# Optimization experiments

Hardware: AMD Instinct MI355X
Metric: run time of the kernel (lower is better)

## Reference

```python
import jax, jax.numpy as jnp
import numpy as np

# Sizes (see shape_source): node irreps 32x0e + 16x1o, edge SH 1x1o,
# messages after concat/filter = 48x0e + 48x1o, MLP 16->64->64->96,
# final equivariant Linear -> 32x0e + 16x1o.
N, E = 50000, 800000
S_IN, V_IN, INV = 32, 16, 16
S_MSG, V_MSG = S_IN + V_IN, S_IN + V_IN  # 48, 48
NFAC = S_MSG + V_MSG                      # 96
S_OUT, V_OUT = 32, 16
SQRT3 = 3.0 ** 0.5


def setup_inputs() -> dict:
    key = jax.random.key(0)
    ks = jax.random.split(key, 12)
    return {
        "edge_src": jax.random.randint(ks[0], (E,), 0, N),
        "edge_dst": jax.random.randint(ks[1], (E,), 0, N),
        "edge_weight_cutoff": jax.random.uniform(ks[2], (E,), dtype=jnp.float32),
        "edge_inv": jax.random.normal(ks[3], (E, INV), dtype=jnp.float32),
        "node_scalars": jax.random.normal(ks[4], (N, S_IN), dtype=jnp.float32),
        "node_vectors": jax.random.normal(ks[5], (N, V_IN, 3), dtype=jnp.float32),
        "edge_sh_vec": jax.random.normal(ks[6], (E, 1, 3), dtype=jnp.float32),
        "W0": jax.random.normal(ks[7], (INV, 64), dtype=jnp.float32),
        "W1": jax.random.normal(ks[8], (64, 64), dtype=jnp.float32),
        "W2": jax.random.normal(ks[9], (64, NFAC), dtype=jnp.float32),
        "WL_s": jax.random.normal(ks[10], (S_MSG, S_OUT), dtype=jnp.float32),
        "WL_v": jax.random.normal(ks[11], (V_MSG, V_OUT), dtype=jnp.float32),
    }


def reference(edge_src, edge_dst, edge_weight_cutoff, edge_inv,
              node_scalars, node_vectors, edge_sh_vec,
              W0, W1, W2, WL_s, WL_v):
    # gather source-node features per edge
    src_s = node_scalars[edge_src]            # [E, 32]
    src_v = node_vectors[edge_src]            # [E, 16, 3]
    ev = edge_sh_vec[:, 0, :]                 # [E, 3] equivariant edge vector (1o)

    # equivariant tensor product (component-normalized CG paths):
    #   0e x 1o -> 1o : scalar * vector
    tp_v = src_s[:, :, None] * edge_sh_vec    # [E, 32, 3]
    #   1o x 1o -> 0e : dot / sqrt(3)   (1e, 2e outputs dropped by the output-irreps filter)
    tp_s = jnp.einsum('eci,ei->ec', src_v, ev) / SQRT3  # [E, 16]

    # concatenate with gathered node features and regroup by irrep
    msg_s = jnp.concatenate([tp_s, src_s], axis=-1)     # [E, 48] (0e block)
    msg_v = jnp.concatenate([tp_v, src_v], axis=1)      # [E, 48, 3] (1o block)

    # edge-conditioned gating MLP on invariant edge features (e3nn-normalized)
    h = jax.nn.silu(edge_inv @ W0 / jnp.sqrt(jnp.float32(INV)))
    h = jax.nn.silu(h @ W1 / jnp.sqrt(jnp.float32(64)))
    fac = h @ W2 / jnp.sqrt(jnp.float32(64))            # [E, 96]

    # elementwise tensor product with scalar factors + smooth cutoff
    g = fac * edge_weight_cutoff[:, None]
    msg_s = msg_s * g[:, :S_MSG]
    msg_v = msg_v * g[:, S_MSG:, None]

    # scatter-sum messages into destination nodes
    out_s = jax.ops.segment_sum(msg_s, edge_dst, num_segments=N)  # [N, 48]
    out_v = jax.ops.segment_sum(msg_v, edge_dst, num_segments=N)  # [N, 48, 3]

    # equivariant Linear to irreps_node_output (fan-in normalized)
    y_s = out_s @ WL_s / jnp.sqrt(jnp.float32(S_MSG))                       # [N, 32]
    y_v = jnp.einsum('eci,co->eoi', out_v, WL_v) / jnp.sqrt(jnp.float32(V_MSG))  # [N, 16, 3]

    # return as contiguous IrrepsArray storage [N, 32 + 16*3]
    return jnp.concatenate([y_s, y_v.reshape(y_v.shape[0], -1)], axis=-1)
```

## Files before the change

kernel.cpp:

```cpp
#include <hip/hip_runtime.h>
#include <hip/hip_fp16.h>
#include <math.h>

constexpr int S_IN = 32, V_IN = 16, INVD = 16;
constexpr int S_MSG = S_IN + V_IN;
constexpr int V_MSG = S_IN + V_IN;
constexpr int NFAC  = S_MSG + V_MSG;
constexpr int S_OUT = 32, V_OUT = 16;
constexpr int OUT_PER_NODE = S_OUT + V_OUT * 3;
constexpr float ISQRT3 = 0.57735026918962576f;
constexpr float ISQ48  = 0.14433756729740643f;

constexpr int PW0 = 0, PW1 = 2560, PW2 = 7168, PWL = 14080, PWTOT = 17536;

typedef _Float16 f16x8 __attribute__((ext_vector_type(8)));
typedef __attribute__((ext_vector_type(4))) float f32x4;

__device__ __forceinline__ float silu_f(float x) {
    return x * __builtin_amdgcn_rcpf(1.0f + __expf(-x));
}
__device__ __forceinline__ unsigned int hpack2(float a, float b) {
    __half2 h = __floats2half2_rn(a, b);
    return *reinterpret_cast<unsigned int*>(&h);
}
__device__ __forceinline__ unsigned short f2h(float f) {
    __half h = __float2half_rn(f);
    return __half_as_ushort(h);
}
__device__ __forceinline__ float h2f(unsigned short u) {
    return __half2float(__ushort_as_half(u));
}
__device__ __forceinline__ float lo16f(unsigned int u) { return h2f((unsigned short)(u & 0xffffu)); }
__device__ __forceinline__ float hi16f(unsigned int u) { return h2f((unsigned short)(u >> 16)); }
__device__ __forceinline__ unsigned int pkmul(unsigned int a, unsigned int b) {
    __half2 ha = *reinterpret_cast<__half2*>(&a);
    __half2 hb = *reinterpret_cast<__half2*>(&b);
    __half2 hc = __hmul2(ha, hb);
    return *reinterpret_cast<unsigned int*>(&hc);
}
__device__ __forceinline__ float2 up2(unsigned int u) {
    __half2 h = *reinterpret_cast<__half2*>(&u);
    return __half22float2(h);
}

__global__ __launch_bounds__(256) void hist_prep(
    const int* __restrict__ edst, int* __restrict__ deg, int E,
    const float* __restrict__ W0, const float* __restrict__ W1,
    const float* __restrict__ W2, const float* __restrict__ WLs,
    const float* __restrict__ WLv,
    const float* __restrict__ ns, const float* __restrict__ nv,
    unsigned short* __restrict__ pW,
    unsigned short* __restrict__ pNS,
    unsigned short* __restrict__ pNV,
    int Nn)
{
    int i = blockIdx.x * 256 + threadIdx.x;
    if (i < E) atomicAdd(&deg[edst[i]], 1);

    int nNS = Nn * 4;
    int nNV = Nn * 6;
    if (i < PWTOT) {
        float v = 0.0f;
        if (i < PW1) {
            int j = i / 40, k = i - 40 * j;
            if (k < INVD) v = W0[k * 64 + j];
        } else if (i < PW2) {
            int t = i - PW1; int j = t / 72, k = t - 72 * j;
            if (k < 64) v = W1[k * 64 + j];
        } else if (i < PWL) {
            int t = i - PW2; int j = t / 72, k = t - 72 * j;
            if (k < 64) v = W2[k * 96 + j];
        } else {
            int t = i - PWL; int j = t / 72, k = t - 72 * j;
            if (k < 48) v = (j < 32) ? WLs[k * S_OUT + j] : WLv[k * V_OUT + (j - 32)];
        }
        pW[i] = f2h(v);
    } else if (i < PWTOT + nNS) {
        int g = i - PWTOT;
        const float4* s4 = reinterpret_cast<const float4*>(ns + (size_t)g * 8);
        float4 a = s4[0], b = s4[1];
        *reinterpret_cast<uint4*>(pNS + (size_t)g * 8) =
            make_uint4(hpack2(a.x, a.y), hpack2(a.z, a.w), hpack2(b.x, b.y), hpack2(b.z, b.w));
    } else if (i < PWTOT + nNS + nNV) {
        int g = i - PWTOT - nNS;
        const float4* s4 = reinterpret_cast<const float4*>(nv + (size_t)g * 8);
        float4 a = s4[0], b = s4[1];
        *reinterpret_cast<uint4*>(pNV + (size_t)g * 8) =
            make_uint4(hpack2(a.x, a.y), hpack2(a.z, a.w), hpack2(b.x, b.y), hpack2(b.z, b.w));
    }
}

__global__ __launch_bounds__(256) void scanA(
    const int* __restrict__ deg, int* __restrict__ bsum, int Nn)
{
    __shared__ int sh[256];
    int i = blockIdx.x * 256 + threadIdx.x;
    sh[threadIdx.x] = (i < Nn) ? deg[i] : 0;
    __syncthreads();
    for (int o = 128; o > 0; o >>= 1) {
        if (threadIdx.x < o) sh[threadIdx.x] += sh[threadIdx.x + o];
        __syncthreads();
    }
    if (threadIdx.x == 0) bsum[blockIdx.x] = sh[0];
}

__global__ __launch_bounds__(1024) void scanB(int* __restrict__ bsum, int nb)
{
    __shared__ int sh[1024];
    int t = threadIdx.x;
    sh[t] = (t < nb) ? bsum[t] : 0;
    __syncthreads();
    for (int o = 1; o < 1024; o <<= 1) {
        int v = (t >= o) ? sh[t - o] : 0;
        __syncthreads();
        sh[t] += v;
        __syncthreads();
    }
    if (t < nb) bsum[t] = (t > 0) ? sh[t - 1] : 0;
}

__global__ __launch_bounds__(256) void scanC(
    const int* __restrict__ deg, const int* __restrict__ bsum,
    int* __restrict__ offs, int* __restrict__ cursor, int Nn, int E)
{
    __shared__ int sh[256];
    int i = blockIdx.x * 256 + threadIdx.x;
    int t = threadIdx.x;
    int v = (i < Nn) ? deg[i] : 0;
    sh[t] = v;
    __syncthreads();
    for (int o = 1; o < 256; o <<= 1) {
        int u = (t >= o) ? sh[t - o] : 0;
        __syncthreads();
        sh[t] += u;
        __syncthreads();
    }
    int excl = sh[t] - v + bsum[blockIdx.x];
    if (i < Nn) { offs[i] = excl; cursor[i] = excl; }
    if (i == Nn - 1) offs[Nn] = E;
}

__global__ __launch_bounds__(256) void scatter_permute(
    const int*   __restrict__ edst,
    const int*   __restrict__ esrc,
    const float* __restrict__ ecut,
    const float* __restrict__ esh,
    const float* __restrict__ einv,
    int* __restrict__ cursor,
    uint4* __restrict__ pedge,
    int E)
{
    int e = blockIdx.x * 256 + threadIdx.x;
    if (e >= E) return;
    int d = edst[e];
    int pos = atomicAdd(&cursor[d], 1);

    const float4* xr = reinterpret_cast<const float4*>(einv + (size_t)e * INVD);
    float4 a = xr[0], b = xr[1], c = xr[2], f = xr[3];
    uint4 r0 = make_uint4(hpack2(a.x, a.y), hpack2(a.z, a.w), hpack2(b.x, b.y), hpack2(b.z, b.w));
    uint4 r1 = make_uint4(hpack2(c.x, c.y), hpack2(c.z, c.w), hpack2(f.x, f.y), hpack2(f.z, f.w));
    uint4 r2 = make_uint4(hpack2(ecut[e], esh[(size_t)e * 3 + 0]),
                          hpack2(esh[(size_t)e * 3 + 1], esh[(size_t)e * 3 + 2]),
                          (unsigned int)esrc[e], (unsigned int)d);

    uint4* dst = pedge + (size_t)pos * 3;
    dst[0] = r0; dst[1] = r1; dst[2] = r2;
}

__global__ __launch_bounds__(256, 3) void edge_mega(
    const uint4* __restrict__ pedge,
    const unsigned short* __restrict__ pW,
    const unsigned short* __restrict__ pNS,
    const unsigned short* __restrict__ pNV,
    float* __restrict__ out,
    int E)
{
    __shared__ __align__(16) unsigned char smem[53760];

    unsigned short* sW0T = (unsigned short*)(smem + 0);
    unsigned short* sW1T = (unsigned short*)(smem + 5120);
    unsigned short* act0 = (unsigned short*)(smem + 14336);
    unsigned short* act1 = (unsigned short*)(smem + 32768);
    unsigned short* sWLT = (unsigned short*)(smem + 5120);
    unsigned short* M    = (unsigned short*)(smem + 14336);
    unsigned short* Fns  = (unsigned short*)(smem + 32768);
    int*            sdst = (int*)(smem + 43008);
    unsigned short* Fnv0 = (unsigned short*)(smem + 43520);
    unsigned short* Fnv1 = (unsigned short*)(smem + 48640);
    unsigned short* Fnv2 = (unsigned short*)(smem + 0);
    float*          redf = (float*)smem;

    const int tid = threadIdx.x;
    const int pbase = blockIdx.x * 128;
    const int p1 = E;

    const int lane = tid & 63;
    const int w    = tid >> 6;
    const int lr   = lane & 15;
    const int lg   = lane >> 4;
    const int eb0  = w * 32 + lr;
    const int eb1  = eb0 + 16;
    const int pA   = pbase + eb0;
    const int pB   = pbase + eb1;

    const uint4 rA2 = pedge[(size_t)(pA < p1 ? pA : p1 - 1) * 3 + 2];
    const uint4 rB2 = pedge[(size_t)(pB < p1 ? pB : p1 - 1) * 3 + 2];
    const float cutA = lo16f(rA2.x);
    const float ev0a = hi16f(rA2.x), ev1a = lo16f(rA2.y), ev2a = hi16f(rA2.y);
    const float cutB = lo16f(rB2.x);
    const float ev0b = hi16f(rB2.x), ev1b = lo16f(rB2.y), ev2b = hi16f(rB2.y);

    const int t2 = tid >> 1, half = tid & 1;
    int dS;
    uint4 pf0, pf1, pf2, pf3, pf4, pf5;
    {
        int pS = pbase + t2; if (pS >= p1) pS = p1 - 1;
        uint4 r2 = pedge[(size_t)pS * 3 + 2];
        int sS = (int)r2.z;
        dS = (int)r2.w;
        if (half == 0) {
            const uint4* nr = reinterpret_cast<const uint4*>(pNS + (size_t)sS * 32);
            pf0 = nr[0]; pf1 = nr[1]; pf2 = nr[2]; pf3 = nr[3];
        } else {
            const uint4* vr = reinterpret_cast<const uint4*>(pNV + (size_t)sS * 48);
            pf0 = vr[0]; pf1 = vr[1]; pf2 = vr[2]; pf3 = vr[3]; pf4 = vr[4]; pf5 = vr[5];
        }
    }

    const uint4* wsrc = reinterpret_cast<const uint4*>(pW);

    {
        uint4* s4 = reinterpret_cast<uint4*>(smem);
        #pragma unroll 2
        for (int i = tid; i < 896; i += 256) s4[i] = wsrc[i];
    }
    if (tid < 128) {
        int p = pbase + tid; if (p >= p1) p = p1 - 1;
        const uint4* rec = pedge + (size_t)p * 3;
        uint4 r0 = rec[0], r1 = rec[1];
        uint4* r4 = reinterpret_cast<uint4*>(&act0[tid * 72]);
        r4[0] = r0;
        r4[1] = r1;
        r4[2] = make_uint4(0u, 0u, 0u, 0u);
        r4[3] = make_uint4(0u, 0u, 0u, 0u);
    }
    __syncthreads();

    const f32x4 zero4 = {0.f, 0.f, 0.f, 0.f};

    {
        f16x8 b0 = *(const f16x8*)&act0[eb0 * 72 + lg * 8];
        f16x8 b1 = *(const f16x8*)&act0[eb1 * 72 + lg * 8];
        #pragma unroll
        for (int jt = 0; jt < 4; jt++) {
            f16x8 a = *(const f16x8*)&sW0T[(jt * 16 + lr) * 40 + lg * 8];
            f32x4 d0 = __builtin_amdgcn_mfma_f32_16x16x32_f16(a, b0, zero4, 0, 0, 0);
            f32x4 d1 = __builtin_amdgcn_mfma_f32_16x16x32_f16(a, b1, zero4, 0, 0, 0);
            unsigned int u0 = hpack2(silu_f(d0[0] * 0.25f), silu_f(d0[1] * 0.25f));
            unsigned int u1 = hpack2(silu_f(d0[2] * 0.25f), silu_f(d0[3] * 0.25f));
            *(uint2*)&act1[eb0 * 72 + jt * 16 + lg * 4] = make_uint2(u0, u1);
            u0 = hpack2(silu_f(d1[0] * 0.25f), silu_f(d1[1] * 0.25f));
            u1 = hpack2(silu_f(d1[2] * 0.25f), silu_f(d1[3] * 0.25f));
            *(uint2*)&act1[eb1 * 72 + jt * 16 + lg * 4] = make_uint2(u0, u1);
        }
    }

    {
        f16x8 b00 = *(const f16x8*)&act1[eb0 * 72 +      lg * 8];
        f16x8 b01 = *(const f16x8*)&act1[eb0 * 72 + 32 + lg * 8];
        f16x8 b10 = *(const f16x8*)&act1[eb1 * 72 +      lg * 8];
        f16x8 b11 = *(const f16x8*)&act1[eb1 * 72 + 32 + lg * 8];
        #pragma unroll
        for (int jt = 0; jt < 4; jt++) {
            f16x8 a0 = *(const f16x8*)&sW1T[(jt * 16 + lr) * 72 +      lg * 8];
            f16x8 a1 = *(const f16x8*)&sW1T[(jt * 16 + lr) * 72 + 32 + lg * 8];
            f32x4 d0 = __builtin_amdgcn_mfma_f32_16x16x32_f16(a0, b00, zero4, 0, 0, 0);
            d0 = __builtin_amdgcn_mfma_f32_16x16x32_f16(a1, b01, d0, 0, 0, 0);
            f32x4 d1 = __builtin_amdgcn_mfma_f32_16x16x32_f16(a0, b10, zero4, 0, 0, 0);
            d1 = __builtin_amdgcn_mfma_f32_16x16x32_f16(a1, b11, d1, 0, 0, 0);
            unsigned int u0 = hpack2(silu_f(d0[0] * 0.125f), silu_f(d0[1] * 0.125f));
            unsigned int u1 = hpack2(silu_f(d0[2] * 0.125f), silu_f(d0[3] * 0.125f));
            *(uint2*)&act0[eb0 * 72 + jt * 16 + lg * 4] = make_uint2(u0, u1);
            u0 = hpack2(silu_f(d1[0] * 0.125f), silu_f(d1[1] * 0.125f));
            u1 = hpack2(silu_f(d1[2] * 0.125f), silu_f(d1[3] * 0.125f));
            *(uint2*)&act0[eb1 * 72 + jt * 16 + lg * 4] = make_uint2(u0, u1);
        }
    }

    __syncthreads();
    {
        uint4* a14 = reinterpret_cast<uint4*>(act1);
        const uint4* w2s = wsrc + 896;
        #pragma unroll 2
        for (int i = tid; i < 864; i += 256) a14[i] = w2s[i];
    }
    __syncthreads();

    float fac0[6][4], fac1[6][4];
    {
        f16x8 b00 = *(const f16x8*)&act0[eb0 * 72 +      lg * 8];
        f16x8 b01 = *(const f16x8*)&act0[eb0 * 72 + 32 + lg * 8];
        f16x8 b10 = *(const f16x8*)&act0[eb1 * 72 +      lg * 8];
        f16x8 b11 = *(const f16x8*)&act0[eb1 * 72 + 32 + lg * 8];
        float K0 = cutA * 0.125f * ISQ48;
        float K1 = cutB * 0.125f * ISQ48;
        #pragma unroll
        for (int jt = 0; jt < 6; jt++) {
            f16x8 a0 = *(const f16x8*)&act1[(jt * 16 + lr) * 72 +      lg * 8];
            f16x8 a1 = *(const f16x8*)&act1[(jt * 16 + lr) * 72 + 32 + lg * 8];
            f32x4 d0 = __builtin_amdgcn_mfma_f32_16x16x32_f16(a0, b00, zero4, 0, 0, 0);
            d0 = __builtin_amdgcn_mfma_f32_16x16x32_f16(a1, b01, d0, 0, 0, 0);
            f32x4 d1 = __builtin_amdgcn_mfma_f32_16x16x32_f16(a0, b10, zero4, 0, 0, 0);
            d1 = __builtin_amdgcn_mfma_f32_16x16x32_f16(a1, b11, d1, 0, 0, 0);
            float s0 = (jt == 0) ? K0 * ISQRT3 : K0;
            float s1 = (jt == 0) ? K1 * ISQRT3 : K1;
            #pragma unroll
            for (int q = 0; q < 4; q++) {
                fac0[jt][q] = d0[q] * s0;
                fac1[jt][q] = d1[q] * s1;
            }
        }
    }
    __syncthreads();

    {
        if (half == 0) {
            uint4* d4 = reinterpret_cast<uint4*>(&Fns[t2 * 40]);
            d4[0] = pf0; d4[1] = pf1;
            uint4* d4b = reinterpret_cast<uint4*>(&Fns[t2 * 40 + 16]);
            d4b[0] = pf2; d4b[1] = pf3;
        } else {
            unsigned int wb[24];
            wb[0]=pf0.x; wb[1]=pf0.y; wb[2]=pf0.z; wb[3]=pf0.w;
            wb[4]=pf1.x; wb[5]=pf1.y; wb[6]=pf1.z; wb[7]=pf1.w;
            wb[8]=pf2.x; wb[9]=pf2.y; wb[10]=pf2.z; wb[11]=pf2.w;
            wb[12]=pf3.x; wb[13]=pf3.y; wb[14]=pf3.z; wb[15]=pf3.w;
            wb[16]=pf4.x; wb[17]=pf4.y; wb[18]=pf4.z; wb[19]=pf4.w;
            wb[20]=pf5.x; wb[21]=pf5.y; wb[22]=pf5.z; wb[23]=pf5.w;
            #pragma unroll
            for (int i = 0; i < 3; i++) {
                unsigned short* FnvI = (i == 0) ? Fnv0 : ((i == 1) ? Fnv1 : Fnv2);
                unsigned int ow[8];
                #pragma unroll
                for (int wd = 0; wd < 8; wd++) {
                    int kLo = 6 * wd + i;
                    int kHi = 6 * wd + 3 + i;
                    unsigned int lo = (kLo & 1) ? (wb[kLo >> 1] >> 16) : (wb[kLo >> 1] & 0xffffu);
                    unsigned int hi = (kHi & 1) ? (wb[kHi >> 1] >> 16) : (wb[kHi >> 1] & 0xffffu);
                    ow[wd] = lo | (hi << 16);
                }
                uint2* d2 = reinterpret_cast<uint2*>(&FnvI[t2 * 20]);
                d2[0] = make_uint2(ow[0], ow[1]);
                d2[1] = make_uint2(ow[2], ow[3]);
                d2[2] = make_uint2(ow[4], ow[5]);
                d2[3] = make_uint2(ow[6], ow[7]);
            }
        }
        uint4* wl4 = reinterpret_cast<uint4*>(sWLT);
        const uint4* wls = wsrc + 896 + 864;
        #pragma unroll 2
        for (int i = tid; i < 432; i += 256) wl4[i] = wls[i];
    }
    __syncthreads();

    uint2 fsrA[2], fsrB[2];
    uint2 fvrA[3], fvrB[3];
    #pragma unroll
    for (int i = 0; i < 3; i++) {
        const unsigned short* FnvI = (i == 0) ? Fnv0 : ((i == 1) ? Fnv1 : Fnv2);
        fvrA[i] = *reinterpret_cast<const uint2*>(&FnvI[eb0 * 20 + lg * 4]);
        fvrB[i] = *reinterpret_cast<const uint2*>(&FnvI[eb1 * 20 + lg * 4]);
    }
    #pragma unroll
    for (int jt = 0; jt < 2; jt++) {
        fsrA[jt] = *reinterpret_cast<const uint2*>(&Fns[eb0 * 40 + jt * 16 + lg * 4]);
        fsrB[jt] = *reinterpret_cast<const uint2*>(&Fns[eb1 * 40 + jt * 16 + lg * 4]);
    }

    uint2 fpA[5], fpB[5];
    #pragma unroll
    for (int jt = 1; jt < 6; jt++) {
        fpA[jt - 1] = make_uint2(hpack2(fac0[jt][0], fac0[jt][1]), hpack2(fac0[jt][2], fac0[jt][3]));
        fpB[jt - 1] = make_uint2(hpack2(fac1[jt][0], fac1[jt][1]), hpack2(fac1[jt][2], fac1[jt][3]));
    }

    {
        float2 a0 = up2(fvrA[0].x), a1 = up2(fvrA[0].y);
        float2 b0 = up2(fvrA[1].x), b1 = up2(fvrA[1].y);
        float2 c0 = up2(fvrA[2].x), c1 = up2(fvrA[2].y);
        float2 d0 = up2(fvrB[0].x), d1 = up2(fvrB[0].y);
        float2 e0 = up2(fvrB[1].x), e1 = up2(fvrB[1].y);
        float2 g0 = up2(fvrB[2].x), g1 = up2(fvrB[2].y);
        float vA[4], vB[4];
        vA[0] = (a0.x*ev0a + b0.x*ev1a + c0.x*ev2a) * fac0[0][0];
        vA[1] = (a0.y*ev0a + b0.y*ev1a + c0.y*ev2a) * fac0[0][1];
        vA[2] = (a1.x*ev0a + b1.x*ev1a + c1.x*ev2a) * fac0[0][2];
        vA[3] = (a1.y*ev0a + b1.y*ev1a + c1.y*ev2a) * fac0[0][3];
        vB[0] = (d0.x*ev0b + e0.x*ev1b + g0.x*ev2b) * fac1[0][0];
        vB[1] = (d0.y*ev0b + e0.y*ev1b + g0.y*ev2b) * fac1[0][1];
        vB[2] = (d1.x*ev0b + e1.x*ev1b + g1.x*ev2b) * fac1[0][2];
        vB[3] = (d1.y*ev0b + e1.y*ev1b + g1.y*ev2b) * fac1[0][3];
        *(uint2*)&M[eb0 * 72 + lg * 4] = make_uint2(hpack2(vA[0], vA[1]), hpack2(vA[2], vA[3]));
        *(uint2*)&M[eb1 * 72 + lg * 4] = make_uint2(hpack2(vB[0], vB[1]), hpack2(vB[2], vB[3]));
    }
    #pragma unroll
    for (int jt = 1; jt < 3; jt++) {
        int c0 = jt * 16 + lg * 4;
        *(uint2*)&M[eb0 * 72 + c0] =
            make_uint2(pkmul(fsrA[jt-1].x, fpA[jt-1].x), pkmul(fsrA[jt-1].y, fpA[jt-1].y));
        *(uint2*)&M[eb1 * 72 + c0] =
            make_uint2(pkmul(fsrB[jt-1].x, fpB[jt-1].x), pkmul(fsrB[jt-1].y, fpB[jt-1].y));
    }
    *(uint2*)&M[eb0 * 72 + 48 + lg * 4] = make_uint2(0u, 0u);
    *(uint2*)&M[eb1 * 72 + 48 + lg * 4] = make_uint2(0u, 0u);

    f32x4 accS[2][2] = {{zero4, zero4}, {zero4, zero4}};
    #pragma unroll
    for (int kt = 0; kt < 2; kt++) {
        f16x8 b0 = *(const f16x8*)&M[eb0 * 72 + kt * 32 + lg * 8];
        f16x8 b1 = *(const f16x8*)&M[eb1 * 72 + kt * 32 + lg * 8];
        #pragma unroll
        for (int ot = 0; ot < 2; ot++) {
            f16x8 a = *(const f16x8*)&sWLT[(ot * 16 + lr) * 72 + kt * 32 + lg * 8];
            accS[0][ot] = __builtin_amdgcn_mfma_f32_16x16x32_f16(a, b0, accS[0][ot], 0, 0, 0);
            accS[1][ot] = __builtin_amdgcn_mfma_f32_16x16x32_f16(a, b1, accS[1][ot], 0, 0, 0);
        }
    }

    #pragma unroll
    for (int jt = 0; jt < 2; jt++) {
        int c0 = jt * 16 + lg * 4;
        *(uint2*)&M[eb0 * 72 + c0] =
            make_uint2(pkmul(fsrA[jt].x, fpA[jt+2].x), pkmul(fsrA[jt].y, fpA[jt+2].y));
        *(uint2*)&M[eb1 * 72 + c0] =
            make_uint2(pkmul(fsrB[jt].x, fpB[jt+2].x), pkmul(fsrB[jt].y, fpB[jt+2].y));
    }
    f32x4 t1A = zero4, t1B = zero4;
    {
        f16x8 b0 = *(const f16x8*)&M[eb0 * 72 + lg * 8];
        f16x8 b1 = *(const f16x8*)&M[eb1 * 72 + lg * 8];
        f16x8 a  = *(const f16x8*)&sWLT[(32 + lr) * 72 + lg * 8];
        t1A = __builtin_amdgcn_mfma_f32_16x16x32_f16(a, b0, t1A, 0, 0, 0);
        t1B = __builtin_amdgcn_mfma_f32_16x16x32_f16(a, b1, t1B, 0, 0, 0);
    }

    float yvA[4][3], yvB[4][3];
    *(uint2*)&M[eb0 * 72 + 16 + lg * 4] = make_uint2(0u, 0u);
    *(uint2*)&M[eb1 * 72 + 16 + lg * 4] = make_uint2(0u, 0u);
    #pragma unroll
    for (int i = 0; i < 3; i++) {
        *(uint2*)&M[eb0 * 72 + lg * 4] =
            make_uint2(pkmul(fvrA[i].x, fpA[4].x), pkmul(fvrA[i].y, fpA[4].y));
        *(uint2*)&M[eb1 * 72 + lg * 4] =
            make_uint2(pkmul(fvrB[i].x, fpB[4].x), pkmul(fvrB[i].y, fpB[4].y));

        f32x4 t2A = zero4, t2B = zero4;
        f16x8 b0 = *(const f16x8*)&M[eb0 * 72 + lg * 8];
        f16x8 b1 = *(const f16x8*)&M[eb1 * 72 + lg * 8];
        f16x8 a  = *(const f16x8*)&sWLT[(32 + lr) * 72 + 32 + lg * 8];
        t2A = __builtin_amdgcn_mfma_f32_16x16x32_f16(a, b0, t2A, 0, 0, 0);
        t2B = __builtin_amdgcn_mfma_f32_16x16x32_f16(a, b1, t2B, 0, 0, 0);

        float evA = (i == 0) ? ev0a : ((i == 1) ? ev1a : ev2a);
        float evB = (i == 0) ? ev0b : ((i == 1) ? ev1b : ev2b);
        #pragma unroll
        for (int q = 0; q < 4; q++) {
            yvA[q][i] = fmaf(evA, t1A[q], t2A[q]);
            yvB[q][i] = fmaf(evB, t1B[q], t2B[q]);
        }
    }

    __syncthreads();

    if (half == 0) sdst[t2] = dS;

    {
        bool okA = (pA < p1), okB = (pB < p1);
        #pragma unroll
        for (int ot = 0; ot < 2; ot++) {
            *(f32x4*)&redf[eb0 * 84 + ot * 16 + lg * 4] = okA ? accS[0][ot] : zero4;
            *(f32x4*)&redf[eb1 * 84 + ot * 16 + lg * 4] = okB ? accS[1][ot] : zero4;
        }
        #pragma unroll
        for (int q = 0; q < 4; q++) {
            int m = lg * 4 + q;
            #pragma unroll
            for (int i = 0; i < 3; i++) {
                redf[eb0 * 84 + 32 + 3 * m + i] = okA ? yvA[q][i] : 0.0f;
                redf[eb1 * 84 + 32 + 3 * m + i] = okB ? yvB[q][i] : 0.0f;
            }
        }
    }
    __syncthreads();

    {
        int base = w * 32;
        int cur = sdst[base];
        float s0 = 0.0f, s1 = 0.0f;
        for (int r = 0; r < 32; r++) {
            int d = sdst[base + r];
            if (d != cur) {
                atomicAdd(&out[(size_t)cur * OUT_PER_NODE + lane], s0);
                if (lane < 16) atomicAdd(&out[(size_t)cur * OUT_PER_NODE + 64 + lane], s1);
                s0 = 0.0f; s1 = 0.0f; cur = d;
            }
            s0 += redf[(base + r) * 84 + lane];
            if (lane < 16) s1 += redf[(base + r) * 84 + 64 + lane];
        }
        atomicAdd(&out[(size_t)cur * OUT_PER_NODE + lane], s0);
        if (lane < 16) atomicAdd(&out[(size_t)cur * OUT_PER_NODE + 64 + lane], s1);
    }
}

extern "C" void kernel_launch(void* const* d_in, const int* in_sizes, int n_in,
                              void* d_out, int out_size, void* d_ws, size_t ws_size,
                              hipStream_t stream) {
    const int*   esrc = (const int*)  d_in[0];
    const int*   edst = (const int*)  d_in[1];
    const float* ecut = (const float*)d_in[2];
    const float* einv = (const float*)d_in[3];
    const float* ns   = (const float*)d_in[4];
    const float* nv   = (const float*)d_in[5];
    const float* esh  = (const float*)d_in[6];
    const float* W0   = (const float*)d_in[7];
    const float* W1   = (const float*)d_in[8];
    const float* W2   = (const float*)d_in[9];
    const float* WLs  = (const float*)d_in[10];
    const float* WLv  = (const float*)d_in[11];
    float* out = (float*)d_out;

    const int E  = in_sizes[0];
    const int Nn = in_sizes[4] / S_IN;
    const int nb = (Nn + 255) / 256;

    size_t int_bytes = (((size_t)(3 * Nn + 1 + nb)) * sizeof(int) + 255) & ~(size_t)255;
    size_t pe_bytes  = ((size_t)E * 48 + 255) & ~(size_t)255;
    size_t pw_bytes  = ((size_t)PWTOT * 2 + 255) & ~(size_t)255;
    size_t ns_bytes  = ((size_t)Nn * 32 * 2 + 255) & ~(size_t)255;
    size_t nv_bytes  = ((size_t)Nn * 48 * 2 + 255) & ~(size_t)255;
    size_t fixed = int_bytes + pe_bytes + pw_bytes + ns_bytes + nv_bytes;

    int eblocks = (E + 255) / 256;

    hipMemsetAsync(out, 0, (size_t)Nn * OUT_PER_NODE * sizeof(float), stream);

    if (ws_size < fixed) return;

    int*            deg    = (int*)d_ws;
    int*            offs   = deg + Nn;
    int*            cursor = offs + Nn + 1;
    int*            bsum   = cursor + Nn;
    uint4*          pedge  = (uint4*)((char*)d_ws + int_bytes);
    unsigned short* pW     = (unsigned short*)((char*)d_ws + int_bytes + pe_bytes);
    unsigned short* pNS    = (unsigned short*)((char*)d_ws + int_bytes + pe_bytes + pw_bytes);
    unsigned short* pNV    = (unsigned short*)((char*)d_ws + int_bytes + pe_bytes + pw_bytes + ns_bytes);

    hipMemsetAsync(deg, 0, (size_t)Nn * sizeof(int), stream);

    int ptotal = PWTOT + Nn * 4 + Nn * 6;
    int hp_blocks = max(eblocks, (ptotal + 255) / 256);
    hist_prep<<<hp_blocks, 256, 0, stream>>>(edst, deg, E, W0, W1, W2, WLs, WLv,
                                             ns, nv, pW, pNS, pNV, Nn);
    scanA<<<nb, 256, 0, stream>>>(deg, bsum, Nn);
    scanB<<<1, 1024, 0, stream>>>(bsum, nb);
    scanC<<<nb, 256, 0, stream>>>(deg, bsum, offs, cursor, Nn, E);
    scatter_permute<<<eblocks, 256, 0, stream>>>(edst, esrc, ecut, esh, einv,
                                                 cursor, pedge, E);

    int mblocks = (E + 127) / 128;
    edge_mega<<<mblocks, 256, 0, stream>>>(pedge, pW, pNS, pNV, out, E);
}
```

Before: 209.6 us.

## Shrink edge_mega shared memory to raise occupancy and reuse one activation buffer

```diff
diff --git a/kernel.cpp b/kernel.cpp
--- a/kernel.cpp
+++ b/kernel.cpp
@@ -121,7 +121,7 @@
 
 __global__ __launch_bounds__(256) void scanC(
     const int* __restrict__ deg, const int* __restrict__ bsum,
-    int* __restrict__ offs, int* __restrict__ cursor, int Nn, int E)
+    int* __restrict__ cursor, int Nn)
 {
     __shared__ int sh[256];
     int i = blockIdx.x * 256 + threadIdx.x;
@@ -136,8 +136,7 @@
         __syncthreads();
     }
     int excl = sh[t] - v + bsum[blockIdx.x];
-    if (i < Nn) { offs[i] = excl; cursor[i] = excl; }
-    if (i == Nn - 1) offs[Nn] = E;
+    if (i < Nn) cursor[i] = excl;
 }
 
 __global__ __launch_bounds__(256) void scatter_permute(
@@ -167,7 +166,7 @@
     dst[0] = r0; dst[1] = r1; dst[2] = r2;
 }
 
-__global__ __launch_bounds__(256, 3) void edge_mega(
+__global__ __launch_bounds__(256, 5) void edge_mega(
     const uint4* __restrict__ pedge,
     const unsigned short* __restrict__ pW,
     const unsigned short* __restrict__ pNS,
@@ -175,20 +174,19 @@
     float* __restrict__ out,
     int E)
 {
-    __shared__ __align__(16) unsigned char smem[53760];
-
-    unsigned short* sW0T = (unsigned short*)(smem + 0);
-    unsigned short* sW1T = (unsigned short*)(smem + 5120);
-    unsigned short* act0 = (unsigned short*)(smem + 14336);
-    unsigned short* act1 = (unsigned short*)(smem + 32768);
-    unsigned short* sWLT = (unsigned short*)(smem + 5120);
-    unsigned short* M    = (unsigned short*)(smem + 14336);
-    unsigned short* Fns  = (unsigned short*)(smem + 32768);
-    int*            sdst = (int*)(smem + 43008);
-    unsigned short* Fnv0 = (unsigned short*)(smem + 43520);
-    unsigned short* Fnv1 = (unsigned short*)(smem + 48640);
-    unsigned short* Fnv2 = (unsigned short*)(smem + 0);
-    float*          redf = (float*)smem;
+    __shared__ __align__(16) unsigned char smem[32768];
+
+    unsigned short* act  = (unsigned short*)(smem + 0);
+    unsigned short* sW0T = (unsigned short*)(smem + 18432);
+    unsigned short* sW1T = (unsigned short*)(smem + 23552);
+    unsigned short* sW2T = (unsigned short*)(smem + 18432);
+    unsigned short* sWLT = (unsigned short*)(smem + 18432);
+    unsigned short* Fns  = (unsigned short*)(smem + 0);
+    unsigned short* Fnv0 = (unsigned short*)(smem + 0);
+    unsigned short* Fnv1 = (unsigned short*)(smem + 5120);
+    unsigned short* Fnv2 = (unsigned short*)(smem + 10240);
+    unsigned short* M    = (unsigned short*)(smem + 0);
+    unsigned short* redh = (unsigned short*)(smem + 0);
 
     const int tid = threadIdx.x;
     const int pbase = blockIdx.x * 128;
@@ -212,25 +210,23 @@
 
     const int t2 = tid >> 1, half = tid & 1;
     int dS;
-    uint4 pf0, pf1, pf2, pf3, pf4, pf5;
+    uint4 pn0, pn1;
+    uint4 pv0, pv1, pv2;
     {
         int pS = pbase + t2; if (pS >= p1) pS = p1 - 1;
         uint4 r2 = pedge[(size_t)pS * 3 + 2];
         int sS = (int)r2.z;
         dS = (int)r2.w;
-        if (half == 0) {
-            const uint4* nr = reinterpret_cast<const uint4*>(pNS + (size_t)sS * 32);
-            pf0 = nr[0]; pf1 = nr[1]; pf2 = nr[2]; pf3 = nr[3];
-        } else {
-            const uint4* vr = reinterpret_cast<const uint4*>(pNV + (size_t)sS * 48);
-            pf0 = vr[0]; pf1 = vr[1]; pf2 = vr[2]; pf3 = vr[3]; pf4 = vr[4]; pf5 = vr[5];
-        }
+        const uint4* nr = reinterpret_cast<const uint4*>(pNS + (size_t)sS * 32);
+        pn0 = nr[half * 2 + 0]; pn1 = nr[half * 2 + 1];
+        const uint4* vr = reinterpret_cast<const uint4*>(pNV + (size_t)sS * 48);
+        pv0 = vr[half * 3 + 0]; pv1 = vr[half * 3 + 1]; pv2 = vr[half * 3 + 2];
     }
 
     const uint4* wsrc = reinterpret_cast<const uint4*>(pW);
 
     {
-        uint4* s4 = reinterpret_cast<uint4*>(smem);
+        uint4* s4 = reinterpret_cast<uint4*>(smem + 18432);
         #pragma unroll 2
         for (int i = tid; i < 896; i += 256) s4[i] = wsrc[i];
     }
@@ -238,7 +234,7 @@
         int p = pbase + tid; if (p >= p1) p = p1 - 1;
         const uint4* rec = pedge + (size_t)p * 3;
         uint4 r0 = rec[0], r1 = rec[1];
-        uint4* r4 = reinterpret_cast<uint4*>(&act0[tid * 72]);
+        uint4* r4 = reinterpret_cast<uint4*>(&act[tid * 72]);
         r4[0] = r0;
         r4[1] = r1;
         r4[2] = make_uint4(0u, 0u, 0u, 0u);
@@ -249,8 +245,8 @@
     const f32x4 zero4 = {0.f, 0.f, 0.f, 0.f};
 
     {
-        f16x8 b0 = *(const f16x8*)&act0[eb0 * 72 + lg * 8];
-        f16x8 b1 = *(const f16x8*)&act0[eb1 * 72 + lg * 8];
+        f16x8 b0 = *(const f16x8*)&act[eb0 * 72 + lg * 8];
+        f16x8 b1 = *(const f16x8*)&act[eb1 * 72 + lg * 8];
         #pragma unroll
         for (int jt = 0; jt < 4; jt++) {
             f16x8 a = *(const f16x8*)&sW0T[(jt * 16 + lr) * 40 + lg * 8];
@@ -258,18 +254,18 @@
             f32x4 d1 = __builtin_amdgcn_mfma_f32_16x16x32_f16(a, b1, zero4, 0, 0, 0);
             unsigned int u0 = hpack2(silu_f(d0[0] * 0.25f), silu_f(d0[1] * 0.25f));
             unsigned int u1 = hpack2(silu_f(d0[2] * 0.25f), silu_f(d0[3] * 0.25f));
-            *(uint2*)&act1[eb0 * 72 + jt * 16 + lg * 4] = make_uint2(u0, u1);
+            *(uint2*)&act[eb0 * 72 + jt * 16 + lg * 4] = make_uint2(u0, u1);
             u0 = hpack2(silu_f(d1[0] * 0.25f), silu_f(d1[1] * 0.25f));
             u1 = hpack2(silu_f(d1[2] * 0.25f), silu_f(d1[3] * 0.25f));
-            *(uint2*)&act1[eb1 * 72 + jt * 16 + lg * 4] = make_uint2(u0, u1);
-        }
-    }
-
-    {
-        f16x8 b00 = *(const f16x8*)&act1[eb0 * 72 +      lg * 8];
-        f16x8 b01 = *(const f16x8*)&act1[eb0 * 72 + 32 + lg * 8];
-        f16x8 b10 = *(const f16x8*)&act1[eb1 * 72 +      lg * 8];
-        f16x8 b11 = *(const f16x8*)&act1[eb1 * 72 + 32 + lg * 8];
+            *(uint2*)&act[eb1 * 72 + jt * 16 + lg * 4] = make_uint2(u0, u1);
+        }
+    }
+
+    {
+        f16x8 b00 = *(const f16x8*)&act[eb0 * 72 +      lg * 8];
+        f16x8 b01 = *(const f16x8*)&act[eb0 * 72 + 32 + lg * 8];
+        f16x8 b10 = *(const f16x8*)&act[eb1 * 72 +      lg * 8];
+        f16x8 b11 = *(const f16x8*)&act[eb1 * 72 + 32 + lg * 8];
         #pragma unroll
         for (int jt = 0; jt < 4; jt++) {
             f16x8 a0 = *(const f16x8*)&sW1T[(jt * 16 + lr) * 72 +      lg * 8];
@@ -280,16 +276,16 @@
             d1 = __builtin_amdgcn_mfma_f32_16x16x32_f16(a1, b11, d1, 0, 0, 0);
             unsigned int u0 = hpack2(silu_f(d0[0] * 0.125f), silu_f(d0[1] * 0.125f));
             unsigned int u1 = hpack2(silu_f(d0[2] * 0.125f), silu_f(d0[3] * 0.125f));
-            *(uint2*)&act0[eb0 * 72 + jt * 16 + lg * 4] = make_uint2(u0, u1);
+            *(uint2*)&act[eb0 * 72 + jt * 16 + lg * 4] = make_uint2(u0, u1);
             u0 = hpack2(silu_f(d1[0] * 0.125f), silu_f(d1[1] * 0.125f));
             u1 = hpack2(silu_f(d1[2] * 0.125f), silu_f(d1[3] * 0.125f));
-            *(uint2*)&act0[eb1 * 72 + jt * 16 + lg * 4] = make_uint2(u0, u1);
-        }
-    }
-
-    __syncthreads();
-    {
-        uint4* a14 = reinterpret_cast<uint4*>(act1);
+            *(uint2*)&act[eb1 * 72 + jt * 16 + lg * 4] = make_uint2(u0, u1);
+        }
+    }
+
+    __syncthreads();
+    {
+        uint4* a14 = reinterpret_cast<uint4*>(smem + 18432);
         const uint4* w2s = wsrc + 896;
         #pragma unroll 2
         for (int i = tid; i < 864; i += 256) a14[i] = w2s[i];
@@ -298,16 +294,16 @@
 
     float fac0[6][4], fac1[6][4];
     {
-        f16x8 b00 = *(const f16x8*)&act0[eb0 * 72 +      lg * 8];
-        f16x8 b01 = *(const f16x8*)&act0[eb0 * 72 + 32 + lg * 8];
-        f16x8 b10 = *(const f16x8*)&act0[eb1 * 72 +      lg * 8];
-        f16x8 b11 = *(const f16x8*)&act0[eb1 * 72 + 32 + lg * 8];
+        f16x8 b00 = *(const f16x8*)&act[eb0 * 72 +      lg * 8];
+        f16x8 b01 = *(const f16x8*)&act[eb0 * 72 + 32 + lg * 8];
+        f16x8 b10 = *(const f16x8*)&act[eb1 * 72 +      lg * 8];
+        f16x8 b11 = *(const f16x8*)&act[eb1 * 72 + 32 + lg * 8];
         float K0 = cutA * 0.125f * ISQ48;
         float K1 = cutB * 0.125f * ISQ48;
         #pragma unroll
         for (int jt = 0; jt < 6; jt++) {
-            f16x8 a0 = *(const f16x8*)&act1[(jt * 16 + lr) * 72 +      lg * 8];
-            f16x8 a1 = *(const f16x8*)&act1[(jt * 16 + lr) * 72 + 32 + lg * 8];
+            f16x8 a0 = *(const f16x8*)&sW2T[(jt * 16 + lr) * 72 +      lg * 8];
+            f16x8 a1 = *(const f16x8*)&sW2T[(jt * 16 + lr) * 72 + 32 + lg * 8];
             f32x4 d0 = __builtin_amdgcn_mfma_f32_16x16x32_f16(a0, b00, zero4, 0, 0, 0);
             d0 = __builtin_amdgcn_mfma_f32_16x16x32_f16(a1, b01, d0, 0, 0, 0);
             f32x4 d1 = __builtin_amdgcn_mfma_f32_16x16x32_f16(a0, b10, zero4, 0, 0, 0);
@@ -324,46 +320,44 @@
     __syncthreads();
 
     {
-        if (half == 0) {
-            uint4* d4 = reinterpret_cast<uint4*>(&Fns[t2 * 40]);
-            d4[0] = pf0; d4[1] = pf1;
-            uint4* d4b = reinterpret_cast<uint4*>(&Fns[t2 * 40 + 16]);
-            d4b[0] = pf2; d4b[1] = pf3;
-        } else {
-            unsigned int wb[24];
-            wb[0]=pf0.x; wb[1]=pf0.y; wb[2]=pf0.z; wb[3]=pf0.w;
-            wb[4]=pf1.x; wb[5]=pf1.y; wb[6]=pf1.z; wb[7]=pf1.w;
-            wb[8]=pf2.x; wb[9]=pf2.y; wb[10]=pf2.z; wb[11]=pf2.w;
-            wb[12]=pf3.x; wb[13]=pf3.y; wb[14]=pf3.z; wb[15]=pf3.w;
-            wb[16]=pf4.x; wb[17]=pf4.y; wb[18]=pf4.z; wb[19]=pf4.w;
-            wb[20]=pf5.x; wb[21]=pf5.y; wb[22]=pf5.z; wb[23]=pf5.w;
-            #pragma unroll
-            for (int i = 0; i < 3; i++) {
-                unsigned short* FnvI = (i == 0) ? Fnv0 : ((i == 1) ? Fnv1 : Fnv2);
-                unsigned int ow[8];
-                #pragma unroll
-                for (int wd = 0; wd < 8; wd++) {
-                    int kLo = 6 * wd + i;
-                    int kHi = 6 * wd + 3 + i;
-                    unsigned int lo = (kLo & 1) ? (wb[kLo >> 1] >> 16) : (wb[kLo >> 1] & 0xffffu);
-                    unsigned int hi = (kHi & 1) ? (wb[kHi >> 1] >> 16) : (wb[kHi >> 1] & 0xffffu);
-                    ow[wd] = lo | (hi << 16);
-                }
-                uint2* d2 = reinterpret_cast<uint2*>(&FnvI[t2 * 20]);
-                d2[0] = make_uint2(ow[0], ow[1]);
-                d2[1] = make_uint2(ow[2], ow[3]);
-                d2[2] = make_uint2(ow[4], ow[5]);
-                d2[3] = make_uint2(ow[6], ow[7]);
-            }
-        }
-        uint4* wl4 = reinterpret_cast<uint4*>(sWLT);
+        uint4* wl4 = reinterpret_cast<uint4*>(smem + 18432);
         const uint4* wls = wsrc + 896 + 864;
         #pragma unroll 2
         for (int i = tid; i < 432; i += 256) wl4[i] = wls[i];
-    }
-    __syncthreads();
-
+
+        uint4* d4 = reinterpret_cast<uint4*>(&Fns[t2 * 40 + half * 16]);
+        d4[0] = pn0; d4[1] = pn1;
+    }
     uint2 fsrA[2], fsrB[2];
+    #pragma unroll
+    for (int jt = 0; jt < 2; jt++) {
+        fsrA[jt] = *reinterpret_cast<const uint2*>(&Fns[eb0 * 40 + jt * 16 + lg * 4]);
+        fsrB[jt] = *reinterpret_cast<const uint2*>(&Fns[eb1 * 40 + jt * 16 + lg * 4]);
+    }
+    __syncthreads();
+
+    {
+        unsigned int wb[12];
+        wb[0]=pv0.x; wb[1]=pv0.y; wb[2]=pv0.z; wb[3]=pv0.w;
+        wb[4]=pv1.x; wb[5]=pv1.y; wb[6]=pv1.z; wb[7]=pv1.w;
+        wb[8]=pv2.x; wb[9]=pv2.y; wb[10]=pv2.z; wb[11]=pv2.w;
+        #pragma unroll
+        for (int i = 0; i < 3; i++) {
+            unsigned short* FnvI = (i == 0) ? Fnv0 : ((i == 1) ? Fnv1 : Fnv2);
+            unsigned int ow[4];
+            #pragma unroll
+            for (int wd = 0; wd < 4; wd++) {
+                int kLo = 6 * wd + i;
+                int kHi = 6 * wd + 3 + i;
+                unsigned int lo = (kLo & 1) ? (wb[kLo >> 1] >> 16) : (wb[kLo >> 1] & 0xffffu);
+                unsigned int hi = (kHi & 1) ? (wb[kHi >> 1] >> 16) : (wb[kHi >> 1] & 0xffffu);
+                ow[wd] = lo | (hi << 16);
+            }
+            uint2* d2 = reinterpret_cast<uint2*>(&FnvI[t2 * 20 + half * 8]);
+            d2[0] = make_uint2(ow[0], ow[1]);
+            d2[1] = make_uint2(ow[2], ow[3]);
+        }
+    }
     uint2 fvrA[3], fvrB[3];
     #pragma unroll
     for (int i = 0; i < 3; i++) {
@@ -371,11 +365,7 @@
         fvrA[i] = *reinterpret_cast<const uint2*>(&FnvI[eb0 * 20 + lg * 4]);
         fvrB[i] = *reinterpret_cast<const uint2*>(&FnvI[eb1 * 20 + lg * 4]);
     }
-    #pragma unroll
-    for (int jt = 0; jt < 2; jt++) {
-        fsrA[jt] = *reinterpret_cast<const uint2*>(&Fns[eb0 * 40 + jt * 16 + lg * 4]);
-        fsrB[jt] = *reinterpret_cast<const uint2*>(&Fns[eb1 * 40 + jt * 16 + lg * 4]);
-    }
+    __syncthreads();
 
     uint2 fpA[5], fpB[5];
     #pragma unroll
@@ -472,40 +462,49 @@
 
     __syncthreads();
 
-    if (half == 0) sdst[t2] = dS;
-
     {
         bool okA = (pA < p1), okB = (pB < p1);
         #pragma unroll
         for (int ot = 0; ot < 2; ot++) {
-            *(f32x4*)&redf[eb0 * 84 + ot * 16 + lg * 4] = okA ? accS[0][ot] : zero4;
-            *(f32x4*)&redf[eb1 * 84 + ot * 16 + lg * 4] = okB ? accS[1][ot] : zero4;
-        }
-        #pragma unroll
-        for (int q = 0; q < 4; q++) {
-            int m = lg * 4 + q;
+            f32x4 sA = okA ? accS[0][ot] : zero4;
+            f32x4 sB = okB ? accS[1][ot] : zero4;
+            *(uint2*)&redh[eb0 * 84 + ot * 16 + lg * 4] =
+                make_uint2(hpack2(sA[0], sA[1]), hpack2(sA[2], sA[3]));
+            *(uint2*)&redh[eb1 * 84 + ot * 16 + lg * 4] =
+                make_uint2(hpack2(sB[0], sB[1]), hpack2(sB[2], sB[3]));
+        }
+        float zA[12], zB[12];
+        #pragma unroll
+        for (int q = 0; q < 4; q++)
             #pragma unroll
             for (int i = 0; i < 3; i++) {
-                redf[eb0 * 84 + 32 + 3 * m + i] = okA ? yvA[q][i] : 0.0f;
-                redf[eb1 * 84 + 32 + 3 * m + i] = okB ? yvB[q][i] : 0.0f;
+                zA[3*q+i] = okA ? yvA[q][i] : 0.0f;
+                zB[3*q+i] = okB ? yvB[q][i] : 0.0f;
             }
-        }
-    }
-    __syncthreads();
+        uint2* dA = (uint2*)&redh[eb0 * 84 + 32 + 12 * lg];
+        dA[0] = make_uint2(hpack2(zA[0], zA[1]),  hpack2(zA[2], zA[3]));
+        dA[1] = make_uint2(hpack2(zA[4], zA[5]),  hpack2(zA[6], zA[7]));
+        dA[2] = make_uint2(hpack2(zA[8], zA[9]),  hpack2(zA[10], zA[11]));
+        uint2* dB = (uint2*)&redh[eb1 * 84 + 32 + 12 * lg];
+        dB[0] = make_uint2(hpack2(zB[0], zB[1]),  hpack2(zB[2], zB[3]));
+        dB[1] = make_uint2(hpack2(zB[4], zB[5]),  hpack2(zB[6], zB[7]));
+        dB[2] = make_uint2(hpack2(zB[8], zB[9]),  hpack2(zB[10], zB[11]));
+    }
 
     {
         int base = w * 32;
-        int cur = sdst[base];
+        int cur = __shfl(dS, 0);
         float s0 = 0.0f, s1 = 0.0f;
         for (int r = 0; r < 32; r++) {
-            int d = sdst[base + r];
+            int d = __shfl(dS, 2 * r);
             if (d != cur) {
                 atomicAdd(&out[(size_t)cur * OUT_PER_NODE + lane], s0);
                 if (lane < 16) atomicAdd(&out[(size_t)cur * OUT_PER_NODE + 64 + lane], s1);
                 s0 = 0.0f; s1 = 0.0f; cur = d;
             }
-            s0 += redf[(base + r) * 84 + lane];
-            if (lane < 16) s1 += redf[(base + r) * 84 + 64 + lane];
+            const unsigned short* row = &redh[(base + r) * 84];
+            s0 += h2f(row[lane]);
+            if (lane < 16) s1 += h2f(row[64 + lane]);
         }
         atomicAdd(&out[(size_t)cur * OUT_PER_NODE + lane], s0);
         if (lane < 16) atomicAdd(&out[(size_t)cur * OUT_PER_NODE + 64 + lane], s1);
@@ -533,7 +532,7 @@
     const int Nn = in_sizes[4] / S_IN;
     const int nb = (Nn + 255) / 256;
 
-    size_t int_bytes = (((size_t)(3 * Nn + 1 + nb)) * sizeof(int) + 255) & ~(size_t)255;
+    size_t int_bytes = (((size_t)(2 * Nn + nb)) * sizeof(int) + 255) & ~(size_t)255;
     size_t pe_bytes  = ((size_t)E * 48 + 255) & ~(size_t)255;
     size_t pw_bytes  = ((size_t)PWTOT * 2 + 255) & ~(size_t)255;
     size_t ns_bytes  = ((size_t)Nn * 32 * 2 + 255) & ~(size_t)255;
@@ -547,8 +546,7 @@
     if (ws_size < fixed) return;
 
     int*            deg    = (int*)d_ws;
-    int*            offs   = deg + Nn;
-    int*            cursor = offs + Nn + 1;
+    int*            cursor = deg + Nn;
     int*            bsum   = cursor + Nn;
     uint4*          pedge  = (uint4*)((char*)d_ws + int_bytes);
     unsigned short* pW     = (unsigned short*)((char*)d_ws + int_bytes + pe_bytes);
@@ -563,7 +561,7 @@
                                              ns, nv, pW, pNS, pNV, Nn);
     scanA<<<nb, 256, 0, stream>>>(deg, bsum, Nn);
     scanB<<<1, 1024, 0, stream>>>(bsum, nb);
-    scanC<<<nb, 256, 0, stream>>>(deg, bsum, offs, cursor, Nn, E);
+    scanC<<<nb, 256, 0, stream>>>(deg, bsum, cursor, Nn);
     scatter_permute<<<eblocks, 256, 0, stream>>>(edst, esrc, ecut, esh, einv,
                                                  cursor, pedge, E);
 
```

Result: slower. 217.4 us (+3.7%).
